# Performance work log

Hardware: AMD Instinct MI355X
Metric: run time of the kernel (lower is better)

## Reference

```python
import jax, jax.numpy as jnp
import numpy as np

K = 3       # deformable kernel size
STRIDE = 2
PAD = 1


def conv2d(x, w, b, stride, pad):
    out = jax.lax.conv_general_dilated(
        x, w, (stride, stride), [(pad, pad), (pad, pad)],
        dimension_numbers=('NCHW', 'OIHW', 'NCHW'))
    return out + b[None, :, None, None]


def setup_inputs() -> dict:
    key = jax.random.key(0)
    ks = jax.random.split(key, 5)
    B, C, H, W, OC = 8, 64, 256, 256, 128
    x = jax.random.normal(ks[0], (B, C, H, W), jnp.float32)
    # offset conv: in_c -> 3*K*K, 3x3, stride 2, pad 1 (small weights ~ trained state)
    offset_w = jax.random.normal(ks[1], (3 * K * K, C, 3, 3), jnp.float32) * 0.05
    offset_b = jax.random.normal(ks[2], (3 * K * K,), jnp.float32) * 0.05
    # main deformable conv weight/bias
    weight = jax.random.normal(ks[3], (OC, C, K, K), jnp.float32) * (1.0 / np.sqrt(C * K * K))
    bias = jax.random.normal(ks[4], (OC,), jnp.float32) * 0.01
    return {'x': x, 'offset_w': offset_w, 'offset_b': offset_b, 'weight': weight, 'bias': bias}


def _bilinear_gather(img, py, px):
    # img: [C, H, W]; py/px: [K2, Ho, Wo] float sampling coords (zero padding outside)
    C, H, W = img.shape
    y0 = jnp.floor(py); x0 = jnp.floor(px)
    y1 = y0 + 1.0;      x1 = x0 + 1.0
    wy1 = py - y0; wy0 = 1.0 - wy1
    wx1 = px - x0; wx0 = 1.0 - wx1

    def corner(yc, xc, wgt):
        valid = (yc >= 0) & (yc <= H - 1) & (xc >= 0) & (xc <= W - 1)
        yi = jnp.clip(yc, 0, H - 1).astype(jnp.int32)
        xi = jnp.clip(xc, 0, W - 1).astype(jnp.int32)
        v = img[:, yi, xi]                      # [C, K2, Ho, Wo]
        return v * (wgt * valid)[None]

    return (corner(y0, x0, wy0 * wx0) + corner(y0, x1, wy0 * wx1)
            + corner(y1, x0, wy1 * wx0) + corner(y1, x1, wy1 * wx1))


def reference(x, offset_w, offset_b, weight, bias):
    B, C, H, W = x.shape
    K2 = K * K
    # offset/mask branch (zero-initialized conv in original; random here = trained state)
    om = conv2d(x, offset_w, offset_b, STRIDE, PAD)       # [B, 3*K2, Ho, Wo]
    off_x, off_y, mask = jnp.split(om, 3, axis=1)         # chunk order from source
    mask = jax.nn.sigmoid(mask)                           # [B, K2, Ho, Wo]
    Ho, Wo = off_x.shape[2], off_x.shape[3]
    # base sampling grid: p0 (output pixel * stride - pad) + kernel point offset + learned offset
    hy = (jnp.arange(Ho) * STRIDE - PAD).astype(jnp.float32)
    wx = (jnp.arange(Wo) * STRIDE - PAD).astype(jnp.float32)
    ky, kx = jnp.meshgrid(jnp.arange(K), jnp.arange(K), indexing='ij')
    ky = ky.reshape(K2).astype(jnp.float32)
    kx = kx.reshape(K2).astype(jnp.float32)
    py = off_y + ky[None, :, None, None] + hy[None, None, :, None]  # [B, K2, Ho, Wo]
    px = off_x + kx[None, :, None, None] + wx[None, None, None, :]
    # bilinear gather per batch element -> [B, C, K2, Ho, Wo]
    sampled = jax.vmap(_bilinear_gather)(x, py, px)
    sampled = sampled * mask[:, None]                     # mask modulation
    w = weight.reshape(weight.shape[0], C, K2)
    out = jnp.einsum('bckhw,ock->bohw', sampled, w) + bias[None, :, None, None]
    return out
```

## Files before the change

### kernel.cpp

```cpp
#include <hip/hip_runtime.h>

typedef unsigned short u16;
typedef __attribute__((ext_vector_type(8))) short bf16x8;
typedef __attribute__((ext_vector_type(8))) unsigned short u16x8;
typedef __attribute__((ext_vector_type(4))) float f32x4;
typedef __attribute__((ext_vector_type(2))) float f32x2;

#define HI 256
#define WI 256
#define CI 64
#define OC 128
#define HO 128
#define WO 128
#define NB 8
#define KC 576
#define KCP 584
#define TW 16

static __device__ __forceinline__ u16 f2bf(float f) {
    union { float f; unsigned u; } v; v.f = f;
    return (u16)((v.u + 0x7FFFu + ((v.u >> 16) & 1u)) >> 16);
}
static __device__ __forceinline__ float bf2f(u16 h) {
    union { unsigned u; float f; } v; v.u = ((unsigned)h) << 16;
    return v.f;
}
static __device__ __forceinline__ f32x2 unpack2(unsigned d) {
    union { unsigned u; float f; } lo, hi;
    lo.u = d << 16;
    hi.u = d & 0xffff0000u;
    f32x2 r; r.x = lo.f; r.y = hi.f;
    return r;
}

__global__ __launch_bounds__(256) void k_wconv(const float* __restrict__ w,
                                               const float* __restrict__ ow,
                                               u16* __restrict__ wbf, u16* __restrict__ wob) {
    int i = blockIdx.x * 256 + threadIdx.x;
    const int NW = OC * KCP;
    if (i < NW) {
        int oc = i / KCP, kc = i - oc * KCP;
        float v = 0.f;
        if (kc < KC) { int k = kc >> 6, c = kc & 63; v = w[oc * KC + c * 9 + k]; }
        wbf[i] = f2bf(v);
    } else {
        int i2 = i - NW;
        if (i2 < 32 * KCP) {
            int oc = i2 / KCP, kc = i2 - oc * KCP;
            float v = 0.f;
            if (oc < 27 && kc < KC) { int k = kc >> 6, c = kc & 63; v = ow[(oc * CI + c) * 9 + k]; }
            wob[i2] = f2bf(v);
        }
    }
}

__global__ __launch_bounds__(256) void k_tr(const float* __restrict__ x, u16* __restrict__ xT, int b0) {
    __shared__ u16 tile[64 * 68];
    const int t = threadIdx.x;
    const int w0 = blockIdx.x * 64;
    const int h  = blockIdx.y;
    const int bz = blockIdx.z;
    const float* xp = x + ((size_t)(b0 + bz) * CI) * (HI * WI) + h * WI + w0;
    #pragma unroll
    for (int i = 0; i < 4; ++i) {
        int c = i * 16 + (t >> 4);
        int w = (t & 15) * 4;
        float4 v = *(const float4*)(xp + (size_t)c * (HI * WI) + w);
        tile[(w + 0) * 68 + c] = f2bf(v.x);
        tile[(w + 1) * 68 + c] = f2bf(v.y);
        tile[(w + 2) * 68 + c] = f2bf(v.z);
        tile[(w + 3) * 68 + c] = f2bf(v.w);
    }
    __syncthreads();
    u16* op = xT + (size_t)bz * (HI * WI * CI) + ((size_t)h * WI + w0) * CI;
    #pragma unroll
    for (int j = 0; j < 4; ++j) {
        int w = j * 16 + (t >> 4);
        int c = (t & 15) * 4;
        *(ushort4*)(op + (size_t)w * CI + c) = *(const ushort4*)&tile[w * 68 + c];
    }
}

__global__ __launch_bounds__(256) void k_off(const u16* __restrict__ xT,
                                             const u16* __restrict__ wob,
                                             const float* __restrict__ ob,
                                             float* __restrict__ om) {
    __shared__ u16 s[32 * KCP];
    __shared__ int atab[288];
    __shared__ float red[2][2][64][4];
    const int t = threadIdx.x;
    const unsigned L = (blockIdx.z * gridDim.y + blockIdx.y) * gridDim.x + blockIdx.x;
    const unsigned nwg = gridDim.x * gridDim.y * gridDim.z;
    const unsigned W = (L & 7u) * (nwg >> 3) + (L >> 3);
    const int wo0 = (W & 3u) * 32;
    const int ho  = (W >> 2) & 127u;
    const int bz  = W >> 9;
    const u16* xb = xT + (size_t)bz * (HI * WI * CI);

    for (int p = t; p < 288; p += 256) {
        int px = p / 9, k = p - px * 9;
        int ky = k / 3, kx = k - ky * 3;
        int y  = ho * 2 - 1 + ky;
        int xx = (wo0 + px) * 2 - 1 + kx;
        bool valid = ((unsigned)y < HI) && ((unsigned)xx < WI);
        atab[p] = valid ? (y * WI + xx) * CI : -1;
    }
    __syncthreads();

    #pragma unroll 3
    for (int it = 0; it < 9; ++it) {
        int idx = it * 256 + t;
        int p = idx >> 3, c8 = idx & 7;
        int a = atab[p];
        u16x8 v = {0, 0, 0, 0, 0, 0, 0, 0};
        if (a >= 0) v = *(const u16x8*)(xb + a + c8 * 8);
        int px = p / 9, k = p - px * 9;
        *(u16x8*)&s[px * KCP + k * 64 + c8 * 8] = v;
    }
    __syncthreads();

    const int lane = t & 63, wv = t >> 6;
    const int q = lane >> 4, l15 = lane & 15;
    const int ph = wv & 1, kh = wv >> 1;
    const u16* sp  = &s[(ph * 16 + l15) * KCP + kh * 288 + q * 8];
    const u16* wp0 = wob + l15 * KCP + kh * 288 + q * 8;
    const u16* wp1 = wob + (16 + l15) * KCP + kh * 288 + q * 8;
    f32x4 acc0 = {0.f, 0.f, 0.f, 0.f}, acc1 = {0.f, 0.f, 0.f, 0.f};
    #pragma unroll
    for (int kt = 0; kt < 9; ++kt) {
        bf16x8 a  = *(const bf16x8*)(sp  + kt * 32);
        bf16x8 b0 = *(const bf16x8*)(wp0 + kt * 32);
        bf16x8 b1 = *(const bf16x8*)(wp1 + kt * 32);
        acc0 = __builtin_amdgcn_mfma_f32_16x16x32_bf16(a, b0, acc0, 0, 0, 0);
        acc1 = __builtin_amdgcn_mfma_f32_16x16x32_bf16(a, b1, acc1, 0, 0, 0);
    }
    if (kh == 1) {
        #pragma unroll
        for (int r = 0; r < 4; ++r) { red[ph][0][lane][r] = acc0[r]; red[ph][1][lane][r] = acc1[r]; }
    }
    __syncthreads();
    if (kh == 0) {
        #pragma unroll
        for (int r = 0; r < 4; ++r) { acc0[r] += red[ph][0][lane][r]; acc1[r] += red[ph][1][lane][r]; }
        const int wo = wo0 + ph * 16 + q * 4;
        float bv0 = ob[l15];
        float* o0 = om + ((size_t)(bz * 27 + l15) * HO + ho) * WO + wo;
        *(float4*)o0 = make_float4(acc0[0] + bv0, acc0[1] + bv0, acc0[2] + bv0, acc0[3] + bv0);
        if (l15 < 11) {
            float bv1 = ob[16 + l15];
            float* o1 = om + ((size_t)(bz * 27 + 16 + l15) * HO + ho) * WO + wo;
            *(float4*)o1 = make_float4(acc1[0] + bv1, acc1[1] + bv1, acc1[2] + bv1, acc1[3] + bv1);
        }
    }
}

__global__ __launch_bounds__(256) void k_main(const u16* __restrict__ xT,
                                              const float* __restrict__ om,
                                              const u16* __restrict__ wbf,
                                              const float* __restrict__ bias,
                                              float* __restrict__ out, int b0) {
    __shared__ u16 s[TW * KCP];
    __shared__ int4   lav[144];
    __shared__ float4 lwv[144];

    const int t = threadIdx.x;
    const unsigned L = (blockIdx.z * gridDim.y + blockIdx.y) * gridDim.x + blockIdx.x;
    const unsigned nwg = gridDim.x * gridDim.y * gridDim.z;
    const unsigned W = (L & 7u) * (nwg >> 3) + (L >> 3);
    const int wo0 = (W & 7u) * TW;
    const int ho  = (W >> 3) & 127u;
    const int bz  = W >> 10;
    const int b = b0 + bz;

    if (t < 144) {
        const int p = t;
        const int px_id = p / 9, k = p - px_id * 9;
        const int wo = wo0 + px_id;
        const size_t base = ((size_t)bz * 27) * (HO * WO) + ho * WO + wo;
        float oxv = om[base + (size_t)k * (HO * WO)];
        float oyv = om[base + (size_t)(9 + k) * (HO * WO)];
        float omm = om[base + (size_t)(18 + k) * (HO * WO)];
        float m = 1.f / (1.f + __expf(-omm));
        float py  = oyv + (float)(k / 3) + (float)(ho * 2 - 1);
        float pxf = oxv + (float)(k % 3) + (float)(wo * 2 - 1);
        float fy = floorf(py), fx = floorf(pxf);
        float wy1 = py - fy, wx1 = pxf - fx;
        float wy0 = 1.f - wy1, wx0 = 1.f - wx1;
        int y0 = (int)fy, x0i = (int)fx;
        int y1 = y0 + 1, x1i = x0i + 1;
        bool vy0 = (y0 >= 0) && (y0 < HI), vy1 = (y1 >= 0) && (y1 < HI);
        bool vx0 = (x0i >= 0) && (x0i < WI), vx1 = (x1i >= 0) && (x1i < WI);
        float w00 = (vy0 && vx0) ? wy0 * wx0 * m : 0.f;
        float w01 = (vy0 && vx1) ? wy0 * wx1 * m : 0.f;
        float w10 = (vy1 && vx0) ? wy1 * wx0 * m : 0.f;
        float w11 = (vy1 && vx1) ? wy1 * wx1 * m : 0.f;
        int y0c = (y0 < 0 ? 0 : (y0 > HI-1 ? HI-1 : y0));
        int y1c = (y1 < 0 ? 0 : (y1 > HI-1 ? HI-1 : y1));
        int x0c = (x0i < 0 ? 0 : (x0i > WI-1 ? WI-1 : x0i));
        int x1c = (x1i < 0 ? 0 : (x1i > WI-1 ? WI-1 : x1i));
        lwv[p] = make_float4(w00, w01, w10, w11);
        lav[p] = make_int4((y0c * WI + x0c) * CI, (y0c * WI + x1c) * CI,
                           (y1c * WI + x0c) * CI, (y1c * WI + x1c) * CI);
    }
    __syncthreads();

    const u16* xb = xT + (size_t)bz * (HI * WI * CI);
    for (int i = t; i < 1152; i += 256) {
        int p = i >> 3;
        int co = (i & 7) * 8;
        int px_id = p / 9, k = p - px_id * 9;
        float4 wv = lwv[p];
        int4   av = lav[p];
        uint4 da = *(const uint4*)(xb + av.x + co);
        uint4 db = *(const uint4*)(xb + av.y + co);
        uint4 dc = *(const uint4*)(xb + av.z + co);
        uint4 dd = *(const uint4*)(xb + av.w + co);
        const unsigned* ua = (const unsigned*)&da;
        const unsigned* ub = (const unsigned*)&db;
        const unsigned* uc = (const unsigned*)&dc;
        const unsigned* ud = (const unsigned*)&dd;
        union { u16x8 v; unsigned u[4]; } r;
        #pragma unroll
        for (int j2 = 0; j2 < 4; ++j2) {
            f32x2 e = wv.x * unpack2(ua[j2]);
            e += wv.y * unpack2(ub[j2]);
            e += wv.z * unpack2(uc[j2]);
            e += wv.w * unpack2(ud[j2]);
            unsigned pk;
            asm("v_cvt_pk_bf16_f32 %0, %1, %2" : "=v"(pk) : "v"(e.x), "v"(e.y));
            r.u[j2] = pk;
        }
        *(u16x8*)&s[px_id * KCP + k * 64 + co] = r.v;
    }
    __syncthreads();

    const int lane = t & 63, wv_ = t >> 6;
    const int q = lane >> 4, l15 = lane & 15;
    const u16* sp  = &s[l15 * KCP + q * 8];
    const int oc0 = wv_ * 32 + l15;
    const int oc1 = oc0 + 16;
    const u16* wp0 = wbf + oc0 * KCP + q * 8;
    const u16* wp1 = wbf + oc1 * KCP + q * 8;
    f32x4 acc0 = {0.f, 0.f, 0.f, 0.f};
    f32x4 acc1 = {0.f, 0.f, 0.f, 0.f};
    #pragma unroll
    for (int kt = 0; kt < 18; ++kt) {
        bf16x8 a  = *(const bf16x8*)(sp  + kt * 32);
        bf16x8 b0 = *(const bf16x8*)(wp0 + kt * 32);
        bf16x8 b1 = *(const bf16x8*)(wp1 + kt * 32);
        acc0 = __builtin_amdgcn_mfma_f32_16x16x32_bf16(a, b0, acc0, 0, 0, 0);
        acc1 = __builtin_amdgcn_mfma_f32_16x16x32_bf16(a, b1, acc1, 0, 0, 0);
    }
    const float bi0 = bias[oc0], bi1 = bias[oc1];
    const int px = q * 4;
    float* op0 = out + (((size_t)b * OC + oc0) * HO + ho) * WO + wo0 + px;
    float* op1 = out + (((size_t)b * OC + oc1) * HO + ho) * WO + wo0 + px;
    *(float4*)op0 = make_float4(acc0[0] + bi0, acc0[1] + bi0, acc0[2] + bi0, acc0[3] + bi0);
    *(float4*)op1 = make_float4(acc1[0] + bi1, acc1[1] + bi1, acc1[2] + bi1, acc1[3] + bi1);
}

extern "C" void kernel_launch(void* const* d_in, const int* in_sizes, int n_in,
                              void* d_out, int out_size, void* d_ws, size_t ws_size,
                              hipStream_t stream) {
    const float* x        = (const float*)d_in[0];
    const float* offset_w = (const float*)d_in[1];
    const float* offset_b = (const float*)d_in[2];
    const float* weight   = (const float*)d_in[3];
    const float* bias     = (const float*)d_in[4];
    float* out = (float*)d_out;

    const size_t xT_full = (size_t)NB * HI * WI * CI * 2;
    const size_t om_full = (size_t)NB * 27 * HO * WO * 4;
    const size_t xT_b    = (size_t)HI * WI * CI * 2;
    const size_t om_b    = (size_t)27 * HO * WO * 4;
    const size_t wsz     = (size_t)(OC + 32) * KCP * 2;
    const int nwb = (int)(((OC + 32) * KCP + 255) / 256);

    if (ws_size >= xT_full + om_full + wsz) {
        u16*   xT  = (u16*)d_ws;
        float* om  = (float*)((char*)d_ws + xT_full);
        u16*   wbf = (u16*)((char*)d_ws + xT_full + om_full);
        u16*   wob = wbf + OC * KCP;
        hipLaunchKernelGGL(k_wconv, dim3(nwb), dim3(256), 0, stream, weight, offset_w, wbf, wob);
        hipLaunchKernelGGL(k_tr,   dim3(4, 256, NB), dim3(256), 0, stream, x, xT, 0);
        hipLaunchKernelGGL(k_off,  dim3(4, 128, NB), dim3(256), 0, stream, xT, wob, offset_b, om);
        hipLaunchKernelGGL(k_main, dim3(8, 128, NB), dim3(256), 0, stream, xT, om, wbf, bias, out, 0);
    } else {
        u16*   xT  = (u16*)d_ws;
        float* om  = (float*)((char*)d_ws + xT_b);
        u16*   wbf = (u16*)((char*)d_ws + xT_b + om_b);
        u16*   wob = wbf + OC * KCP;
        hipLaunchKernelGGL(k_wconv, dim3(nwb), dim3(256), 0, stream, weight, offset_w, wbf, wob);
        for (int b = 0; b < NB; ++b) {
            hipLaunchKernelGGL(k_tr,   dim3(4, 256, 1), dim3(256), 0, stream, x, xT, b);
            hipLaunchKernelGGL(k_off,  dim3(4, 128, 1), dim3(256), 0, stream, xT, wob, offset_b, om);
            hipLaunchKernelGGL(k_main, dim3(8, 128, 1), dim3(256), 0, stream, xT, om, wbf, bias, out, b);
        }
    }
}
```

Baseline: 364.9 us.

## Widen main-kernel tile to 32 pixels with 512 threads and prefetch weights

The deformable main kernel now handles 32 output pixels per workgroup, using 512 threads (8 waves split into two pixel halves times four output-channel groups) instead of 16 pixels with 256 threads. Each workgroup covers twice the work and the gather loop is restructured to fit. The MFMA loop also double-buffers the weight-operand loads two K-steps ahead to hide global load latency. This raises LDS use and register pressure (launch bounds 512,6), which can reduce occupancy.

```diff
diff --git a/kernel.cpp b/kernel.cpp
--- a/kernel.cpp
+++ b/kernel.cpp
@@ -15,7 +15,7 @@
 #define NB 8
 #define KC 576
 #define KCP 584
-#define TW 16
+#define TW 32
 
 static __device__ __forceinline__ u16 f2bf(float f) {
     union { float f; unsigned u; } v; v.f = f;
@@ -154,25 +154,25 @@
     }
 }
 
-__global__ __launch_bounds__(256) void k_main(const u16* __restrict__ xT,
-                                              const float* __restrict__ om,
-                                              const u16* __restrict__ wbf,
-                                              const float* __restrict__ bias,
-                                              float* __restrict__ out, int b0) {
+__global__ __launch_bounds__(512, 6) void k_main(const u16* __restrict__ xT,
+                                                 const float* __restrict__ om,
+                                                 const u16* __restrict__ wbf,
+                                                 const float* __restrict__ bias,
+                                                 float* __restrict__ out, int b0) {
     __shared__ u16 s[TW * KCP];
-    __shared__ int4   lav[144];
-    __shared__ float4 lwv[144];
+    __shared__ int4   lav[288];
+    __shared__ float4 lwv[288];
 
     const int t = threadIdx.x;
     const unsigned L = (blockIdx.z * gridDim.y + blockIdx.y) * gridDim.x + blockIdx.x;
     const unsigned nwg = gridDim.x * gridDim.y * gridDim.z;
     const unsigned W = (L & 7u) * (nwg >> 3) + (L >> 3);
-    const int wo0 = (W & 7u) * TW;
-    const int ho  = (W >> 3) & 127u;
-    const int bz  = W >> 10;
+    const int wo0 = (W & 3u) * TW;
+    const int ho  = (W >> 2) & 127u;
+    const int bz  = W >> 9;
     const int b = b0 + bz;
 
-    if (t < 144) {
+    if (t < 288) {
         const int p = t;
         const int px_id = p / 9, k = p - px_id * 9;
         const int wo = wo0 + px_id;
@@ -205,7 +205,7 @@
     __syncthreads();
 
     const u16* xb = xT + (size_t)bz * (HI * WI * CI);
-    for (int i = t; i < 1152; i += 256) {
+    auto gb = [&](int i) {
         int p = i >> 3;
         int co = (i & 7) * 8;
         int px_id = p / 9, k = p - px_id * 9;
@@ -231,30 +231,41 @@
             r.u[j2] = pk;
         }
         *(u16x8*)&s[px_id * KCP + k * 64 + co] = r.v;
-    }
+    };
+    #pragma unroll 2
+    for (int it = 0; it < 4; ++it) gb(it * 512 + t);
+    if (t < 256) gb(2048 + t);
     __syncthreads();
 
     const int lane = t & 63, wv_ = t >> 6;
     const int q = lane >> 4, l15 = lane & 15;
-    const u16* sp  = &s[l15 * KCP + q * 8];
-    const int oc0 = wv_ * 32 + l15;
+    const int ph = wv_ >> 2, og = wv_ & 3;
+    const u16* sp  = &s[(ph * 16 + l15) * KCP + q * 8];
+    const int oc0 = og * 32 + l15;
     const int oc1 = oc0 + 16;
     const u16* wp0 = wbf + oc0 * KCP + q * 8;
     const u16* wp1 = wbf + oc1 * KCP + q * 8;
     f32x4 acc0 = {0.f, 0.f, 0.f, 0.f};
     f32x4 acc1 = {0.f, 0.f, 0.f, 0.f};
+    bf16x8 b0b[2], b1b[2];
+    b0b[0] = *(const bf16x8*)(wp0);
+    b1b[0] = *(const bf16x8*)(wp1);
+    b0b[1] = *(const bf16x8*)(wp0 + 32);
+    b1b[1] = *(const bf16x8*)(wp1 + 32);
     #pragma unroll
     for (int kt = 0; kt < 18; ++kt) {
-        bf16x8 a  = *(const bf16x8*)(sp  + kt * 32);
-        bf16x8 b0 = *(const bf16x8*)(wp0 + kt * 32);
-        bf16x8 b1 = *(const bf16x8*)(wp1 + kt * 32);
-        acc0 = __builtin_amdgcn_mfma_f32_16x16x32_bf16(a, b0, acc0, 0, 0, 0);
-        acc1 = __builtin_amdgcn_mfma_f32_16x16x32_bf16(a, b1, acc1, 0, 0, 0);
+        bf16x8 a = *(const bf16x8*)(sp + kt * 32);
+        acc0 = __builtin_amdgcn_mfma_f32_16x16x32_bf16(a, b0b[kt & 1], acc0, 0, 0, 0);
+        acc1 = __builtin_amdgcn_mfma_f32_16x16x32_bf16(a, b1b[kt & 1], acc1, 0, 0, 0);
+        if (kt + 2 < 18) {
+            b0b[kt & 1] = *(const bf16x8*)(wp0 + (kt + 2) * 32);
+            b1b[kt & 1] = *(const bf16x8*)(wp1 + (kt + 2) * 32);
+        }
     }
     const float bi0 = bias[oc0], bi1 = bias[oc1];
-    const int px = q * 4;
-    float* op0 = out + (((size_t)b * OC + oc0) * HO + ho) * WO + wo0 + px;
-    float* op1 = out + (((size_t)b * OC + oc1) * HO + ho) * WO + wo0 + px;
+    const int wo = wo0 + ph * 16 + q * 4;
+    float* op0 = out + (((size_t)b * OC + oc0) * HO + ho) * WO + wo;
+    float* op1 = out + (((size_t)b * OC + oc1) * HO + ho) * WO + wo;
     *(float4*)op0 = make_float4(acc0[0] + bi0, acc0[1] + bi0, acc0[2] + bi0, acc0[3] + bi0);
     *(float4*)op1 = make_float4(acc1[0] + bi1, acc1[1] + bi1, acc1[2] + bi1, acc1[3] + bi1);
 }
@@ -284,7 +295,7 @@
         hipLaunchKernelGGL(k_wconv, dim3(nwb), dim3(256), 0, stream, weight, offset_w, wbf, wob);
         hipLaunchKernelGGL(k_tr,   dim3(4, 256, NB), dim3(256), 0, stream, x, xT, 0);
         hipLaunchKernelGGL(k_off,  dim3(4, 128, NB), dim3(256), 0, stream, xT, wob, offset_b, om);
-        hipLaunchKernelGGL(k_main, dim3(8, 128, NB), dim3(256), 0, stream, xT, om, wbf, bias, out, 0);
+        hipLaunchKernelGGL(k_main, dim3(4, 128, NB), dim3(512), 0, stream, xT, om, wbf, bias, out, 0);
     } else {
         u16*   xT  = (u16*)d_ws;
         float* om  = (float*)((char*)d_ws + xT_b);
@@ -294,7 +305,7 @@
         for (int b = 0; b < NB; ++b) {
             hipLaunchKernelGGL(k_tr,   dim3(4, 256, 1), dim3(256), 0, stream, x, xT, b);
             hipLaunchKernelGGL(k_off,  dim3(4, 128, 1), dim3(256), 0, stream, xT, wob, offset_b, om);
-            hipLaunchKernelGGL(k_main, dim3(8, 128, 1), dim3(256), 0, stream, xT, om, wbf, bias, out, b);
-        }
-    }
-}
+            hipLaunchKernelGGL(k_main, dim3(4, 128, 1), dim3(512), 0, stream, xT, om, wbf, bias, out, b);
+        }
+    }
+}
```

After: 364.2 us. No clear change (-0.2%).
